# Performance work log

Measured on AMD Instinct MI355X. Metric: run time of the kernel, lower is better.

Reference implementation:

```python
import jax, jax.numpy as jnp
import numpy as np

NUM_ADC_P = 8           # num_of_adc_p
L_TILDE = 64            # num_samples_L_tilde
DENSE_L = 1024          # params.dense_sampling_L
GAUSS_STD = 10.0        # params.gaussian_sampling_std


def setup_inputs() -> dict:
    key = jax.random.key(0)
    kx, = jax.random.split(key, 1)
    B = 16384
    x = jax.random.normal(kx, (B, NUM_ADC_P * DENSE_L), dtype=jnp.float32)
    # learned sample positions, init = linspace(0, L, L_tilde+2)[1:-1]
    start = np.linspace(0.0, DENSE_L, L_TILDE + 2, dtype=np.float64)[1:-1]
    weight = jnp.asarray(start, dtype=jnp.float32)
    return {"x": x, "weight": weight}


def reference(x, weight):
    B = x.shape[0]
    dt = x.dtype
    t = jnp.arange(1, DENSE_L + 1, dtype=dt)                      # [L]
    # Gaussian weighting matrix shared across all ADC channels: [L, L_tilde]
    W = jnp.exp(-((t[:, None] - weight[None, :].astype(dt)) ** 2) / (GAUSS_STD ** 2))
    xb = x.reshape(B, NUM_ADC_P, DENSE_L)                         # [B, P, L]
    out = jnp.einsum('bpl,lk->bpk', xb, W)                        # [B, P, L_tilde]
    return out.reshape(B, NUM_ADC_P * L_TILDE)
```

## Files before the change

kernel.cpp:

```cpp
#include <hip/hip_runtime.h>
#include <hip/hip_bf16.h>

#define NUM_ADC_P 8
#define DENSE_L   1024
#define L_TILDE   64

typedef __attribute__((ext_vector_type(8))) short  short8;
typedef __attribute__((ext_vector_type(4))) float  float4v;

__global__ void build_w(const float* __restrict__ weight,
                        __hip_bfloat16* __restrict__ wt) {
    const int n = blockIdx.x;
    const float wn = weight[n];
    for (int k = threadIdx.x; k < DENSE_L; k += blockDim.x) {
        const float t = (float)(k + 1);
        const float d = t - wn;
        const float v = expf(-d * d * (1.0f / 100.0f));
        wt[n * DENSE_L + k] = __float2bfloat16(v);
    }
}

__device__ __forceinline__ short cvt_bf16(float f) {
    unsigned u = __builtin_bit_cast(unsigned, f);
    u += 0x7fffu + ((u >> 16) & 1u);
    return (short)(u >> 16);
}

__device__ __forceinline__ short8 cvt8(float4v a, float4v b) {
    short8 r;
    r[0] = cvt_bf16(a[0]); r[1] = cvt_bf16(a[1]);
    r[2] = cvt_bf16(a[2]); r[3] = cvt_bf16(a[3]);
    r[4] = cvt_bf16(b[0]); r[5] = cvt_bf16(b[1]);
    r[6] = cvt_bf16(b[2]); r[7] = cvt_bf16(b[3]);
    return r;
}

__global__ __launch_bounds__(256, 4)
void sampling_gemm(const float* __restrict__ x,
                   const __hip_bfloat16* __restrict__ wt,
                   float* __restrict__ out) {
    const int lane = threadIdx.x & 63;
    const int wave = threadIdx.x >> 6;
    const int r    = lane & 15;
    const int q    = lane >> 4;

    const long m0 = (long)blockIdx.x * 128 + (long)wave * 32;

    const float* a0 = x + (m0 + r) * DENSE_L + q * 8;
    const float* a1 = a0 + 16 * DENSE_L;
    const short* w0 = (const short*)wt + r * DENSE_L + q * 8;

    float4v acc[2][4];
    #pragma unroll
    for (int i = 0; i < 2; ++i)
        #pragma unroll
        for (int j = 0; j < 4; ++j)
            acc[i][j] = (float4v){0.f, 0.f, 0.f, 0.f};

    for (int kk = 0; kk < DENSE_L; kk += 32) {
        const float4v af0a = *(const float4v*)(a0 + kk);
        const float4v af0b = *(const float4v*)(a0 + kk + 4);
        const float4v af1a = *(const float4v*)(a1 + kk);
        const float4v af1b = *(const float4v*)(a1 + kk + 4);

        short8 bf[4];
        #pragma unroll
        for (int ns = 0; ns < 4; ++ns)
            bf[ns] = *(const short8*)(w0 + ns * 16 * DENSE_L + kk);

        const short8 af0 = cvt8(af0a, af0b);
        const short8 af1 = cvt8(af1a, af1b);

        #pragma unroll
        for (int ns = 0; ns < 4; ++ns) {
            acc[0][ns] = __builtin_amdgcn_mfma_f32_16x16x32_bf16(af0, bf[ns], acc[0][ns], 0, 0, 0);
            acc[1][ns] = __builtin_amdgcn_mfma_f32_16x16x32_bf16(af1, bf[ns], acc[1][ns], 0, 0, 0);
        }
    }

    #pragma unroll
    for (int ms = 0; ms < 2; ++ms) {
        #pragma unroll
        for (int ns = 0; ns < 4; ++ns) {
            #pragma unroll
            for (int rr = 0; rr < 4; ++rr) {
                out[(m0 + ms * 16 + q * 4 + rr) * L_TILDE + ns * 16 + r] = acc[ms][ns][rr];
            }
        }
    }
}

extern "C" void kernel_launch(void* const* d_in, const int* in_sizes, int n_in,
                              void* d_out, int out_size, void* d_ws, size_t ws_size,
                              hipStream_t stream) {
    const float* x      = (const float*)d_in[0];
    const float* weight = (const float*)d_in[1];
    float* out          = (float*)d_out;
    __hip_bfloat16* wt  = (__hip_bfloat16*)d_ws;

    const int M = in_sizes[0] / DENSE_L;
    const int grid = M / 128;

    build_w<<<64, 256, 0, stream>>>(weight, wt);
    sampling_gemm<<<grid, 256, 0, stream>>>(x, wt, out);
}
```

Baseline: 740.2 us.

## Skip near-zero Gaussian K-blocks, prefetch x nontemporally, use packed bf16 conversion

Computes, per 16-column output group, the range of K blocks where the Gaussian weights are non-negligible, and skips MFMAs and weight loads outside that range. The x row loads become software-prefetched one iteration ahead using nontemporal loads, conversion uses packed bf16 intrinsics, and outputs use nontemporal stores. The kernel remains bound by streaming all of x (each row is still read in full), so the MFMA skipping mainly cuts compute and weight traffic. Skipping depends on weights staying within the computed window (±~49 cutoff), which assumes bf16-negligible tails.

Measured after the change: 703.7 us. 4.9% less time.

```diff
diff --git a/kernel.cpp b/kernel.cpp
--- a/kernel.cpp
+++ b/kernel.cpp
@@ -8,36 +8,49 @@
 typedef __attribute__((ext_vector_type(8))) short  short8;
 typedef __attribute__((ext_vector_type(4))) float  float4v;
 
+
 __global__ void build_w(const float* __restrict__ weight,
-                        __hip_bfloat16* __restrict__ wt) {
+                        __hip_bfloat16* __restrict__ wt,
+                        int* __restrict__ ranges) {
     const int n = blockIdx.x;
     const float wn = weight[n];
     for (int k = threadIdx.x; k < DENSE_L; k += blockDim.x) {
         const float t = (float)(k + 1);
         const float d = t - wn;
-        const float v = expf(-d * d * (1.0f / 100.0f));
-        wt[n * DENSE_L + k] = __float2bfloat16(v);
+        wt[n * DENSE_L + k] = __float2bfloat16(expf(-d * d * 0.01f));
+    }
+    if (blockIdx.x == 0 && threadIdx.x < 4) {
+        const int g = threadIdx.x;
+        float wmin = 1e30f, wmax = -1e30f;
+        for (int j = 0; j < 16; ++j) {
+            const float w = weight[g * 16 + j];
+            wmin = fminf(wmin, w);
+            wmax = fmaxf(wmax, w);
+        }
+        int klo = (int)floorf(wmin) - 49; if (klo < 0) klo = 0;
+        int khi = (int)ceilf(wmax) + 48;  if (khi > DENSE_L - 1) khi = DENSE_L - 1;
+        ranges[2 * g]     = klo >> 5;
+        ranges[2 * g + 1] = khi >> 5;
     }
 }
 
-__device__ __forceinline__ short cvt_bf16(float f) {
-    unsigned u = __builtin_bit_cast(unsigned, f);
-    u += 0x7fffu + ((u >> 16) & 1u);
-    return (short)(u >> 16);
+__device__ __forceinline__ short8 cvt8(float4v a, float4v b) {
+    union { short8 s; __hip_bfloat162 h[4]; } u;
+    u.h[0] = __float22bfloat162_rn(make_float2(a[0], a[1]));
+    u.h[1] = __float22bfloat162_rn(make_float2(a[2], a[3]));
+    u.h[2] = __float22bfloat162_rn(make_float2(b[0], b[1]));
+    u.h[3] = __float22bfloat162_rn(make_float2(b[2], b[3]));
+    return u.s;
 }
 
-__device__ __forceinline__ short8 cvt8(float4v a, float4v b) {
-    short8 r;
-    r[0] = cvt_bf16(a[0]); r[1] = cvt_bf16(a[1]);
-    r[2] = cvt_bf16(a[2]); r[3] = cvt_bf16(a[3]);
-    r[4] = cvt_bf16(b[0]); r[5] = cvt_bf16(b[1]);
-    r[6] = cvt_bf16(b[2]); r[7] = cvt_bf16(b[3]);
-    return r;
+__device__ __forceinline__ float4v ldnt(const float* p) {
+    return __builtin_nontemporal_load((const float4v*)p);
 }
 
 __global__ __launch_bounds__(256, 4)
 void sampling_gemm(const float* __restrict__ x,
                    const __hip_bfloat16* __restrict__ wt,
+                   const int* __restrict__ ranges,
                    float* __restrict__ out) {
     const int lane = threadIdx.x & 63;
     const int wave = threadIdx.x >> 6;
@@ -50,6 +63,11 @@
     const float* a1 = a0 + 16 * DENSE_L;
     const short* w0 = (const short*)wt + r * DENSE_L + q * 8;
 
+    const int lo0 = ranges[0], hi0 = ranges[1];
+    const int lo1 = ranges[2], hi1 = ranges[3];
+    const int lo2 = ranges[4], hi2 = ranges[5];
+    const int lo3 = ranges[6], hi3 = ranges[7];
+
     float4v acc[2][4];
     #pragma unroll
     for (int i = 0; i < 2; ++i)
@@ -57,25 +75,42 @@
         for (int j = 0; j < 4; ++j)
             acc[i][j] = (float4v){0.f, 0.f, 0.f, 0.f};
 
-    for (int kk = 0; kk < DENSE_L; kk += 32) {
-        const float4v af0a = *(const float4v*)(a0 + kk);
-        const float4v af0b = *(const float4v*)(a0 + kk + 4);
-        const float4v af1a = *(const float4v*)(a1 + kk);
-        const float4v af1b = *(const float4v*)(a1 + kk + 4);
+    float4v c0a = ldnt(a0), c0b = ldnt(a0 + 4);
+    float4v c1a = ldnt(a1), c1b = ldnt(a1 + 4);
 
-        short8 bf[4];
-        #pragma unroll
-        for (int ns = 0; ns < 4; ++ns)
-            bf[ns] = *(const short8*)(w0 + ns * 16 * DENSE_L + kk);
+    for (int kk = 0; kk < 32; ++kk) {
+        const int kn = (kk + 1) & 31;
+        const float4v n0a = ldnt(a0 + kn * 32);
+        const float4v n0b = ldnt(a0 + kn * 32 + 4);
+        const float4v n1a = ldnt(a1 + kn * 32);
+        const float4v n1b = ldnt(a1 + kn * 32 + 4);
 
-        const short8 af0 = cvt8(af0a, af0b);
-        const short8 af1 = cvt8(af1a, af1b);
+        const short8 af0 = cvt8(c0a, c0b);
+        const short8 af1 = cvt8(c1a, c1b);
+        const short* wk = w0 + kk * 32;
 
-        #pragma unroll
-        for (int ns = 0; ns < 4; ++ns) {
-            acc[0][ns] = __builtin_amdgcn_mfma_f32_16x16x32_bf16(af0, bf[ns], acc[0][ns], 0, 0, 0);
-            acc[1][ns] = __builtin_amdgcn_mfma_f32_16x16x32_bf16(af1, bf[ns], acc[1][ns], 0, 0, 0);
+        if (kk >= lo0 && kk <= hi0) {
+            const short8 b = *(const short8*)(wk);
+            acc[0][0] = __builtin_amdgcn_mfma_f32_16x16x32_bf16(af0, b, acc[0][0], 0, 0, 0);
+            acc[1][0] = __builtin_amdgcn_mfma_f32_16x16x32_bf16(af1, b, acc[1][0], 0, 0, 0);
         }
+        if (kk >= lo1 && kk <= hi1) {
+            const short8 b = *(const short8*)(wk + 16 * DENSE_L);
+            acc[0][1] = __builtin_amdgcn_mfma_f32_16x16x32_bf16(af0, b, acc[0][1], 0, 0, 0);
+            acc[1][1] = __builtin_amdgcn_mfma_f32_16x16x32_bf16(af1, b, acc[1][1], 0, 0, 0);
+        }
+        if (kk >= lo2 && kk <= hi2) {
+            const short8 b = *(const short8*)(wk + 32 * DENSE_L);
+            acc[0][2] = __builtin_amdgcn_mfma_f32_16x16x32_bf16(af0, b, acc[0][2], 0, 0, 0);
+            acc[1][2] = __builtin_amdgcn_mfma_f32_16x16x32_bf16(af1, b, acc[1][2], 0, 0, 0);
+        }
+        if (kk >= lo3 && kk <= hi3) {
+            const short8 b = *(const short8*)(wk + 48 * DENSE_L);
+            acc[0][3] = __builtin_amdgcn_mfma_f32_16x16x32_bf16(af0, b, acc[0][3], 0, 0, 0);
+            acc[1][3] = __builtin_amdgcn_mfma_f32_16x16x32_bf16(af1, b, acc[1][3], 0, 0, 0);
+        }
+
+        c0a = n0a; c0b = n0b; c1a = n1a; c1b = n1b;
     }
 
     #pragma unroll
@@ -84,7 +119,9 @@
         for (int ns = 0; ns < 4; ++ns) {
             #pragma unroll
             for (int rr = 0; rr < 4; ++rr) {
-                out[(m0 + ms * 16 + q * 4 + rr) * L_TILDE + ns * 16 + r] = acc[ms][ns][rr];
+                __builtin_nontemporal_store(
+                    acc[ms][ns][rr],
+                    out + (m0 + ms * 16 + q * 4 + rr) * L_TILDE + ns * 16 + r);
             }
         }
     }
@@ -97,10 +134,11 @@
     const float* weight = (const float*)d_in[1];
     float* out          = (float*)d_out;
     __hip_bfloat16* wt  = (__hip_bfloat16*)d_ws;
+    int* ranges         = (int*)((char*)d_ws + 64 * DENSE_L * sizeof(__hip_bfloat16));
 
     const int M = in_sizes[0] / DENSE_L;
     const int grid = M / 128;
 
-    build_w<<<64, 256, 0, stream>>>(weight, wt);
-    sampling_gemm<<<grid, 256, 0, stream>>>(x, wt, out);
+    build_w<<<64, 256, 0, stream>>>(weight, wt, ranges);
+    sampling_gemm<<<grid, 256, 0, stream>>>(x, wt, ranges, out);
 }
```
